# Optimization experiments

Measured on AMD Instinct MI355X. Metric: run time of the kernel, lower is better.

Reference implementation:

```python
import jax, jax.numpy as jnp
import numpy as np

H = 16          # query heads
HKV = 4         # kv heads
DK = 128        # head_qk_dim
DV = 128        # head_v_dim
HID = 2048
KSZ = 4         # conv kernel size
EPS = 1e-5
NORMALIZER = 16.0


def _causal_dwconv_silu(x, w):
    # x: (B,S,C), w: (C,K). Causal depthwise conv then SiLU.
    B, S, C = x.shape
    K = w.shape[1]
    xp = jnp.pad(x, ((0, 0), (K - 1, 0), (0, 0)))
    y = jnp.zeros_like(x)
    for i in range(K):  # K=4, tiny fixed loop
        y = y + w[:, i] * xp[:, i:i + S, :]
    return jax.nn.silu(y)


def _l2norm(x, eps=1e-6):
    return x * jax.lax.rsqrt(jnp.sum(x * x, axis=-1, keepdims=True) + eps)


def setup_inputs() -> dict:
    key = jax.random.key(0)
    ks = jax.random.split(key, 8)
    B, S = 2, 2048
    qkv_dim = H * DK + HKV * DK + HKV * DV  # 3072
    s = lambda fan_in: 1.0 / np.sqrt(fan_in)
    return {
        "hidden_states": jax.random.normal(ks[0], (B, S, HID), jnp.float32),
        "qkv_w": jax.random.uniform(ks[1], (qkv_dim, HID), jnp.float32, -s(HID), s(HID)),
        "g_w": jax.random.uniform(ks[2], (H * DV, HID), jnp.float32, -s(HID), s(HID)),
        "b_w": jax.random.uniform(ks[3], (H, HID), jnp.float32, -s(HID), s(HID)),
        "gk_w": jax.random.uniform(ks[4], (H, HID), jnp.float32, -s(HID), s(HID)),
        "conv_w": jax.random.uniform(ks[5], (qkv_dim, KSZ), jnp.float32, -s(KSZ), s(KSZ)),
        "out_norm_w": jnp.ones((DV,), jnp.float32),
        "o_w": jax.random.uniform(ks[6], (HID, H * DV), jnp.float32, -s(H * DV), s(H * DV)),
    }


def reference(hidden_states, qkv_w, g_w, b_w, gk_w, conv_w, out_norm_w, o_w):
    x = hidden_states
    B, S, _ = x.shape
    grp = H // HKV

    qkv = x @ qkv_w.T                                   # (B,S,3072)
    qkv = _causal_dwconv_silu(qkv, conv_w)
    q, k, v = jnp.split(qkv, [H * DK, H * DK + HKV * DK], axis=-1)
    q = q.reshape(B, S, H, DK)
    k = k.reshape(B, S, HKV, DK)
    v = v.reshape(B, S, HKV, DV)
    # GQA expansion
    k = jnp.repeat(k, grp, axis=2)                      # (B,S,H,DK)
    v = jnp.repeat(v, grp, axis=2)                      # (B,S,H,DV)

    # q/k L2 norm + scale
    q = _l2norm(q) * (DK ** -0.5)
    k = _l2norm(k)

    # decay gate (logsigmoid, log-space), write strength beta
    g_log = jax.nn.log_sigmoid(x @ gk_w.T) / NORMALIZER  # (B,S,H)
    alpha = jnp.exp(g_log)
    beta = jax.nn.sigmoid(x @ b_w.T)                     # (B,S,H)

    # gated delta rule: S_t = a_t*S_{t-1} + k_t (x) beta_t*(v_t - k_t @ (a_t*S_{t-1}))
    def step(Sstate, inp):
        q_t, k_t, v_t, a_t, b_t = inp                    # (B,H,*)
        Sstate = Sstate * a_t[..., None, None]           # (B,H,DK,DV)
        v_pred = jnp.einsum('bhk,bhkv->bhv', k_t, Sstate)
        delta = (v_t - v_pred) * b_t[..., None]
        Sstate = Sstate + jnp.einsum('bhk,bhv->bhkv', k_t, delta)
        o_t = jnp.einsum('bhk,bhkv->bhv', q_t, Sstate)
        return Sstate, o_t

    tfirst = lambda a: jnp.moveaxis(a, 1, 0)             # (S,B,H,...)
    S0 = jnp.zeros((B, H, DK, DV), x.dtype)
    _, o = jax.lax.scan(step, S0, (tfirst(q), tfirst(k), tfirst(v), tfirst(alpha), tfirst(beta)))
    o = jnp.moveaxis(o, 0, 1)                            # (B,S,H,DV)

    # gated per-head RMSNorm then output projection
    g = (x @ g_w.T).reshape(B, S, H, DV)
    o = o * jax.lax.rsqrt(jnp.mean(o * o, axis=-1, keepdims=True) + EPS) * out_norm_w
    o = o * jax.nn.silu(g)
    return (o.reshape(B, S, H * DV)) @ o_w.T
```

## Files before the change

kernel.cpp:

```cpp
#include <hip/hip_runtime.h>
#include <math.h>

#define S_LEN 2048
#define BATCH 2
#define NH 16
#define NKV 4
#define DKQ 128
#define DVV 128
#define HID 2048
#define QKV_DIM 3072
#define M_TOK 4096

typedef _Float16 halfx8 __attribute__((ext_vector_type(8)));
typedef _Float16 halfx4 __attribute__((ext_vector_type(4)));
typedef float floatx4 __attribute__((ext_vector_type(4)));

#define AS1 __attribute__((address_space(1)))
#define AS3 __attribute__((address_space(3)))
#define GLD16(gp, lp) __builtin_amdgcn_global_load_lds((AS1 const void*)(gp), (AS3 void*)(lp), 16, 0, 0)
#define MFMA16(a, b, c) __builtin_amdgcn_mfma_f32_16x16x32_f16(a, b, c, 0, 0, 0)

#define PA_STRIDE 81920

__device__ __forceinline__ float sigmoidf_(float x) { return 1.f / (1.f + __expf(-x)); }

__global__ __launch_bounds__(256) void cvt_f16(const float* __restrict__ in,
                                               _Float16* __restrict__ out, int n8) {
  int i = blockIdx.x * 256 + threadIdx.x;
  if (i >= n8) return;
  const float4* p = (const float4*)in;
  float4 a = p[2 * (size_t)i], b = p[2 * (size_t)i + 1];
  halfx8 o;
  o[0] = (_Float16)a.x; o[1] = (_Float16)a.y; o[2] = (_Float16)a.z; o[3] = (_Float16)a.w;
  o[4] = (_Float16)b.x; o[5] = (_Float16)b.y; o[6] = (_Float16)b.z; o[7] = (_Float16)b.w;
  *(halfx8*)(out + (size_t)i * 8) = o;
}

__global__ __launch_bounds__(256) void gemm_bt_f16(const _Float16* __restrict__ A,
                                                   const _Float16* __restrict__ B,
                                                   float* __restrict__ C,
                                                   int M, int N, int K) {
  __shared__ _Float16 As[128 * 32];
  __shared__ _Float16 Bs[128 * 32];
  int bm = blockIdx.y * 128, bn = blockIdx.x * 128;
  int tid = threadIdx.x;
  int w = tid >> 6, l = tid & 63;
  int wm = (w & 1) * 64, wn = (w >> 1) * 64;
  int lrow = l & 15, lk8 = (l >> 4) * 8;

  floatx4 zero = {0.f, 0.f, 0.f, 0.f};
  floatx4 acc[4][4];
#pragma unroll
  for (int i = 0; i < 4; ++i)
#pragma unroll
    for (int j = 0; j < 4; ++j) acc[i][j] = zero;

  const _Float16* ga = A + (size_t)(bm + (tid >> 2)) * K + (tid & 3) * 8;
  const _Float16* gb = B + (size_t)(bn + (tid >> 2)) * K + (tid & 3) * 8;
  _Float16* lA = As + w * 512;
  _Float16* lB = Bs + w * 512;

  for (int k0 = 0; k0 < K; k0 += 32) {
    GLD16(ga + k0, lA);
    GLD16(ga + k0 + (size_t)64 * K, lA + 2048);
    GLD16(gb + k0, lB);
    GLD16(gb + k0 + (size_t)64 * K, lB + 2048);
    __syncthreads();
    halfx8 af[4], bf_[4];
#pragma unroll
    for (int mi = 0; mi < 4; ++mi)
      af[mi] = *(const halfx8*)&As[(wm + mi * 16 + lrow) * 32 + lk8];
#pragma unroll
    for (int ni = 0; ni < 4; ++ni)
      bf_[ni] = *(const halfx8*)&Bs[(wn + ni * 16 + lrow) * 32 + lk8];
#pragma unroll
    for (int mi = 0; mi < 4; ++mi)
#pragma unroll
      for (int ni = 0; ni < 4; ++ni)
        acc[mi][ni] = MFMA16(af[mi], bf_[ni], acc[mi][ni]);
    __syncthreads();
  }
  int r0 = (l >> 4) * 4;
#pragma unroll
  for (int mi = 0; mi < 4; ++mi)
#pragma unroll
    for (int ni = 0; ni < 4; ++ni) {
      int col = bn + wn + ni * 16 + lrow;
#pragma unroll
      for (int r = 0; r < 4; ++r)
        C[(size_t)(bm + wm + mi * 16 + r0 + r) * N + col] = acc[mi][ni][r];
    }
}

__global__ __launch_bounds__(256) void gkb_kernel(const float* __restrict__ X,
                                                  const float* __restrict__ gk_w,
                                                  const float* __restrict__ b_w,
                                                  float* __restrict__ glog,
                                                  float* __restrict__ be) {
  __shared__ float xs[16][260];
  __shared__ float ws[32][260];
  int tid = threadIdx.x;
  int m0 = blockIdx.x * 16;
  int tl = tid >> 4, n0 = tid & 15;
  float acc0 = 0.f, acc1 = 0.f;
  for (int k0 = 0; k0 < HID; k0 += 256) {
#pragma unroll
    for (int i = 0; i < 4; ++i) {
      int F = i * 256 + tid;
      int r = F >> 6, c4 = (F & 63) * 4;
      *(float4*)&xs[r][c4] = *(const float4*)&X[(size_t)(m0 + r) * HID + k0 + c4];
    }
#pragma unroll
    for (int i = 0; i < 8; ++i) {
      int F = i * 256 + tid;
      int r = F >> 6, c4 = (F & 63) * 4;
      const float* src = (r < 16) ? (gk_w + (size_t)r * HID) : (b_w + (size_t)(r - 16) * HID);
      *(float4*)&ws[r][c4] = *(const float4*)&src[k0 + c4];
    }
    __syncthreads();
#pragma unroll 16
    for (int k = 0; k < 256; k += 4) {
      float4 a = *(const float4*)&xs[tl][k];
      float4 w0 = *(const float4*)&ws[n0][k];
      float4 w1 = *(const float4*)&ws[n0 + 16][k];
      acc0 += a.x * w0.x + a.y * w0.y + a.z * w0.z + a.w * w0.w;
      acc1 += a.x * w1.x + a.y * w1.y + a.z * w1.z + a.w * w1.w;
    }
    __syncthreads();
  }
  int m = m0 + tl, b = m >> 11, s = m & (S_LEN - 1);
  float z = acc0;
  float ls = (z >= 0.f) ? -log1pf(expf(-z)) : (z - log1pf(expf(z)));
  size_t oi = (size_t)(b * NH + n0) * S_LEN + s;
  glog[oi] = ls * 0.0625f;
  be[oi] = sigmoidf_(acc1);
}

__global__ __launch_bounds__(256) void conv_kernel(const float* __restrict__ qkv,
                                                   const float* __restrict__ conv_w,
                                                   float* __restrict__ qn,
                                                   float* __restrict__ kn,
                                                   float* __restrict__ vn) {
  __shared__ float ys[QKV_DIM];
  __shared__ float sc[20];
  int m = blockIdx.x;
  int b = m >> 11, s = m & (S_LEN - 1);
  int tid = threadIdx.x;
  for (int c = tid; c < QKV_DIM; c += 256) {
    float acc = 0.f;
#pragma unroll
    for (int i = 0; i < 4; ++i) {
      int si = s - 3 + i;
      if (si >= 0) acc += conv_w[c * 4 + i] * qkv[(size_t)(b * S_LEN + si) * QKV_DIM + c];
    }
    ys[c] = acc * (1.f / (1.f + __expf(-acc)));
  }
  __syncthreads();
  int wv = tid >> 6, lane = tid & 63;
  for (int ch = wv; ch < 20; ch += 4) {
    int base = (ch < 16) ? ch * 128 : 2048 + (ch - 16) * 128;
    float x0 = ys[base + lane], x1 = ys[base + 64 + lane];
    float ss = x0 * x0 + x1 * x1;
#pragma unroll
    for (int off = 1; off < 64; off <<= 1) ss += __shfl_xor(ss, off);
    float scale = rsqrtf(ss + 1e-6f);
    if (ch < 16) scale *= 0.08838834764831845f;
    if (lane == 0) sc[ch] = scale;
  }
  __syncthreads();
  for (int c = tid; c < 2048; c += 256) {
    int h = c >> 7, d = c & 127;
    qn[((size_t)(b * NH + h) * S_LEN + s) * DKQ + d] = ys[c] * sc[h];
  }
  for (int c = tid; c < 512; c += 256) {
    int j = c >> 7, d = c & 127;
    kn[((size_t)(b * NKV + j) * S_LEN + s) * DKQ + d] = ys[2048 + c] * sc[16 + j];
    vn[((size_t)(b * NKV + j) * S_LEN + s) * DVV + d] = ys[2560 + c];
  }
}

__global__ __launch_bounds__(256, 2) void phaseA_kernel(const float* __restrict__ qn,
                                                        const float* __restrict__ kn,
                                                        const float* __restrict__ vn,
                                                        const float* __restrict__ glog,
                                                        const float* __restrict__ be,
                                                        char* __restrict__ pout,
                                                        float* __restrict__ obuf) {
  __shared__ char smem[80128] __attribute__((aligned(16)));
  _Float16* kh = (_Float16*)smem;
  _Float16* qh = (_Float16*)(smem + 22528);
  float*    LT = (float*)(smem + 45056);
  _Float16* Ph = (_Float16*)(smem + 67584);
  float*    sc_c    = (float*)(smem + 78848);
  float*    sc_beta = sc_c + 64;
  float*    sc_gam  = sc_c + 128;
  float*    sc_bg   = sc_c + 192;
  float*    sc_gcr  = sc_c + 256;
  _Float16* Dt = (_Float16*)smem;
  _Float16* Wt = (_Float16*)(smem + 22528);
  _Float16* Kt = (_Float16*)(smem + 45056);

  int u = blockIdx.x;
  int bh = u >> 5, ch = u & 31;
  int t0 = ch * 64;
  int b = bh >> 4, h = bh & 15, kvh = h >> 2;
  const float* qb = qn + ((size_t)bh * S_LEN + t0) * DKQ;
  const float* kb = kn + (((size_t)(b * NKV + kvh)) * S_LEN + t0) * DKQ;
  const float* vb = vn + (((size_t)(b * NKV + kvh)) * S_LEN + t0) * DVV;
  const float* gl = glog + (size_t)bh * S_LEN + t0;
  const float* ber = be + (size_t)bh * S_LEN + t0;
  char* base = pout + (size_t)u * PA_STRIDE;
  _Float16* M_out = (_Float16*)base;
  _Float16* E_out = (_Float16*)(base + 32768);
  _Float16* B_out = (_Float16*)(base + 49152);
  float* ob = obuf + ((size_t)bh * S_LEN + t0) * DVV;

  int tid = threadIdx.x;
  if (tid < 64) {
    float x = gl[tid];
#pragma unroll
    for (int off = 1; off < 64; off <<= 1) {
      float y = __shfl_up(x, off);
      if (tid >= off) x += y;
    }
    sc_c[tid] = x;
  }
#pragma unroll
  for (int i = 0; i < 8; ++i) {
    int idx = i * 256 + tid;
    int t = idx >> 5, d4 = (idx & 31) * 4;
    float4 kv4 = *(const float4*)&kb[(size_t)t * DKQ + d4];
    float4 qv4 = *(const float4*)&qb[(size_t)t * DKQ + d4];
    _Float16* kd = &kh[t * 152 + d4];
    kd[0] = (_Float16)kv4.x; kd[1] = (_Float16)kv4.y; kd[2] = (_Float16)kv4.z; kd[3] = (_Float16)kv4.w;
    _Float16* qd = &qh[t * 152 + d4];
    qd[0] = (_Float16)qv4.x; qd[1] = (_Float16)qv4.y; qd[2] = (_Float16)qv4.z; qd[3] = (_Float16)qv4.w;
  }
  __syncthreads();
  if (tid < 64) {
    float c = sc_c[tid], c63 = sc_c[63];
    float gam = __expf(c);
    float bet = ber[tid];
    sc_gam[tid] = gam; sc_beta[tid] = bet; sc_bg[tid] = bet * gam;
    sc_gcr[tid] = __expf(c63 - c);
  }
  __syncthreads();

  float z[64];
  {
    const float* src = (tid < 128) ? vb : kb;
    const float* mult = (tid < 128) ? sc_beta : sc_bg;
    int col = tid & 127;
#pragma unroll
    for (int t = 0; t < 64; ++t) z[t] = mult[t] * src[(size_t)t * 128 + col];
  }

  int w = tid >> 6, l = tid & 63;
  int lr = l & 15, lk8 = (l >> 4) * 8, q4 = (l >> 4) * 4;
  floatx4 acc[8];
#pragma unroll
  for (int i = 0; i < 8; ++i) acc[i] = (floatx4){0.f, 0.f, 0.f, 0.f};
#pragma unroll
  for (int job = 0; job < 8; ++job) {
    int j2 = w * 8 + job;
    int tm = (j2 & 15) >> 2, tn = j2 & 3;
    const _Float16* Ar = (j2 < 16) ? kh : qh;
#pragma unroll
    for (int kk = 0; kk < 4; ++kk) {
      halfx8 af = *(const halfx8*)&Ar[(tm * 16 + lr) * 152 + kk * 32 + lk8];
      halfx8 bf = *(const halfx8*)&kh[(tn * 16 + lr) * 152 + kk * 32 + lk8];
      acc[job] = MFMA16(af, bf, acc[job]);
    }
  }
#pragma unroll
  for (int job = 0; job < 8; ++job) {
    int j2 = w * 8 + job;
    int tm = (j2 & 15) >> 2, tn = j2 & 3;
    int jcol = tn * 16 + lr;
    float cj = sc_c[jcol];
#pragma unroll
    for (int r = 0; r < 4; ++r) {
      int trow = tm * 16 + q4 + r;
      float val = acc[job][r] * __expf(sc_c[trow] - cj);
      if (j2 < 16) {
        LT[jcol * 68 + trow] = (jcol < trow) ? sc_beta[trow] * val : 0.f;
      } else {
        Ph[trow * 88 + jcol] = (_Float16)((jcol <= trow) ? val : 0.f);
      }
    }
  }
  __syncthreads();

#pragma unroll
  for (int t = 0; t < 64; ++t) {
    float zt = z[t];
    const int start = ((t + 1) >> 2) << 2;
#pragma unroll
    for (int t2 = start; t2 < 64; t2 += 4) {
      float4 lv = *(const float4*)&LT[t * 68 + t2];
      z[t2 + 0] -= lv.x * zt;
      z[t2 + 1] -= lv.y * zt;
      z[t2 + 2] -= lv.z * zt;
      z[t2 + 3] -= lv.w * zt;
    }
  }
  floatx4 Eacc[8];
#pragma unroll
  for (int ni = 0; ni < 8; ++ni)
#pragma unroll
    for (int r = 0; r < 4; ++r) {
      int trow = w * 16 + q4 + r;
      Eacc[ni][r] = sc_gam[trow] * (float)qh[trow * 152 + ni * 16 + lr];
    }
  __syncthreads();

  {
    int d = tid >> 1, tb = (tid & 1) * 32;
#pragma unroll
    for (int j = 0; j < 4; ++j) {
      halfx8 kv;
#pragma unroll
      for (int r = 0; r < 8; ++r) {
        int t = tb + j * 8 + r;
        kv[r] = (_Float16)(sc_gcr[t] * (float)kh[t * 152 + d]);
      }
      *(halfx8*)&Kt[d * 88 + tb + j * 8] = kv;
    }
  }
  if (tid >= 128) {
    int col = tid & 127;
#pragma unroll
    for (int t = 0; t < 64; t += 8) {
      halfx8 wv;
#pragma unroll
      for (int r = 0; r < 8; ++r) wv[r] = (_Float16)(-z[t + r]);
      *(halfx8*)&Wt[col * 88 + t] = wv;
    }
  }
  __syncthreads();
  if (tid < 128) {
    int col = tid & 127;
#pragma unroll
    for (int t = 0; t < 64; t += 8) {
      halfx8 dv;
#pragma unroll
      for (int r = 0; r < 8; ++r) dv[r] = (_Float16)z[t + r];
      *(halfx8*)&Dt[col * 88 + t] = dv;
    }
  }
  __syncthreads();

  floatx4 Macc[2][8], Bacc[2][8], Oacc[8];
  float gC = __expf(sc_c[63]);
#pragma unroll
  for (int mi = 0; mi < 2; ++mi)
#pragma unroll
    for (int ni = 0; ni < 8; ++ni) {
#pragma unroll
      for (int r = 0; r < 4; ++r)
        Macc[mi][ni][r] = ((w * 32 + mi * 16 + q4 + r) == (ni * 16 + lr)) ? gC : 0.f;
      Bacc[mi][ni] = (floatx4){0.f, 0.f, 0.f, 0.f};
    }
#pragma unroll
  for (int ni = 0; ni < 8; ++ni) Oacc[ni] = (floatx4){0.f, 0.f, 0.f, 0.f};
#pragma unroll
  for (int ks = 0; ks < 2; ++ks) {
    halfx8 ka0 = *(const halfx8*)&Kt[(w * 32 + lr) * 88 + ks * 32 + lk8];
    halfx8 ka1 = *(const halfx8*)&Kt[(w * 32 + 16 + lr) * 88 + ks * 32 + lk8];
    halfx8 pa = *(const halfx8*)&Ph[(w * 16 + lr) * 88 + ks * 32 + lk8];
#pragma unroll
    for (int ni = 0; ni < 8; ++ni) {
      halfx8 wb = *(const halfx8*)&Wt[(ni * 16 + lr) * 88 + ks * 32 + lk8];
      halfx8 db = *(const halfx8*)&Dt[(ni * 16 + lr) * 88 + ks * 32 + lk8];
      Macc[0][ni] = MFMA16(ka0, wb, Macc[0][ni]);
      Macc[1][ni] = MFMA16(ka1, wb, Macc[1][ni]);
      Bacc[0][ni] = MFMA16(ka0, db, Bacc[0][ni]);
      Bacc[1][ni] = MFMA16(ka1, db, Bacc[1][ni]);
      Eacc[ni] = MFMA16(pa, wb, Eacc[ni]);
      Oacc[ni] = MFMA16(pa, db, Oacc[ni]);
    }
  }
#pragma unroll
  for (int mi = 0; mi < 2; ++mi)
#pragma unroll
    for (int ni = 0; ni < 8; ++ni)
#pragma unroll
      for (int r = 0; r < 4; ++r) {
        int row = w * 32 + mi * 16 + q4 + r;
        M_out[row * 128 + ni * 16 + lr] = (_Float16)Macc[mi][ni][r];
        B_out[ni * 2048 + row * 16 + lr] = (_Float16)Bacc[mi][ni][r];
      }
#pragma unroll
  for (int ni = 0; ni < 8; ++ni)
#pragma unroll
    for (int r = 0; r < 4; ++r) {
      int trow = w * 16 + q4 + r;
      E_out[trow * 128 + ni * 16 + lr] = (_Float16)Eacc[ni][r];
      ob[(size_t)trow * 128 + ni * 16 + lr] = Oacc[ni][r];
    }
}

__global__ __launch_bounds__(256, 1) void phaseB_kernel(const char* __restrict__ pin,
                                                        float* __restrict__ obuf) {
  __shared__ _Float16 Mh[2][128 * 152];
  __shared__ _Float16 Eh[2][64 * 152];
  __shared__ _Float16 St[2][16 * 152];

  int bh = blockIdx.x & 31, vg = blockIdx.x >> 5;
  int tid = threadIdx.x, w = tid >> 6, l = tid & 63;
  int lr = l & 15, lk8 = (l >> 4) * 8, q4 = (l >> 4) * 4;
  const char* ub0 = pin + (size_t)(bh * 32) * PA_STRIDE;
  float* ob_base = obuf + (size_t)bh * S_LEN * DVV + vg * 16;

  float4 Mr[8], Er[4];
  float Bc[2][4], Oc[4], Bn[2][4], On[4];

  {
    const float4* Mg = (const float4*)ub0;
    const float4* Eg = (const float4*)(ub0 + 32768);
    const _Float16* Bg = (const _Float16*)(ub0 + 49152) + vg * 2048;
#pragma unroll
    for (int j = 0; j < 8; ++j) Mr[j] = Mg[j * 256 + tid];
#pragma unroll
    for (int j = 0; j < 4; ++j) Er[j] = Eg[j * 256 + tid];
#pragma unroll
    for (int mi = 0; mi < 2; ++mi)
#pragma unroll
      for (int r = 0; r < 4; ++r)
        Bc[mi][r] = (float)Bg[(w * 32 + mi * 16 + q4 + r) * 16 + lr];
#pragma unroll
    for (int r = 0; r < 4; ++r)
      Oc[r] = ob_base[(size_t)(w * 16 + q4 + r) * DVV + lr];
#pragma unroll
    for (int j = 0; j < 8; ++j) {
      int n = j * 256 + tid;
      *(float4*)&Mh[0][(n >> 4) * 152 + (n & 15) * 8] = Mr[j];
    }
#pragma unroll
    for (int j = 0; j < 4; ++j) {
      int n = j * 256 + tid;
      *(float4*)&Eh[0][(n >> 4) * 152 + (n & 15) * 8] = Er[j];
    }
    halfx4 z4;
    z4[0] = (_Float16)0.f; z4[1] = (_Float16)0.f; z4[2] = (_Float16)0.f; z4[3] = (_Float16)0.f;
#pragma unroll
    for (int mi = 0; mi < 2; ++mi)
      *(halfx4*)&St[0][lr * 152 + w * 32 + mi * 16 + q4] = z4;
  }
  asm volatile("s_waitcnt lgkmcnt(0)" ::: "memory");

  for (int c = 0; c < 32; ++c) {
    __builtin_amdgcn_s_barrier();
    int cur = c & 1, nxt = cur ^ 1;
    bool have = (c + 1) < 32;
    if (have) {
      const char* un = ub0 + (size_t)(c + 1) * PA_STRIDE;
      const float4* Mg = (const float4*)un;
      const float4* Eg = (const float4*)(un + 32768);
      const _Float16* Bg = (const _Float16*)(un + 49152) + vg * 2048;
#pragma unroll
      for (int j = 0; j < 8; ++j) Mr[j] = Mg[j * 256 + tid];
#pragma unroll
      for (int j = 0; j < 4; ++j) Er[j] = Eg[j * 256 + tid];
#pragma unroll
      for (int mi = 0; mi < 2; ++mi)
#pragma unroll
        for (int r = 0; r < 4; ++r)
          Bn[mi][r] = (float)Bg[(w * 32 + mi * 16 + q4 + r) * 16 + lr];
#pragma unroll
      for (int r = 0; r < 4; ++r)
        On[r] = ob_base[(size_t)((c + 1) * 64 + w * 16 + q4 + r) * DVV + lr];
    }
    floatx4 Sn0 = {Bc[0][0], Bc[0][1], Bc[0][2], Bc[0][3]};
    floatx4 Sn1 = {Bc[1][0], Bc[1][1], Bc[1][2], Bc[1][3]};
    floatx4 Oa = {Oc[0], Oc[1], Oc[2], Oc[3]};
#pragma unroll
    for (int ks = 0; ks < 4; ++ks) {
      halfx8 sf = *(const halfx8*)&St[cur][lr * 152 + ks * 32 + lk8];
      halfx8 ma0 = *(const halfx8*)&Mh[cur][(w * 32 + lr) * 152 + ks * 32 + lk8];
      halfx8 ma1 = *(const halfx8*)&Mh[cur][(w * 32 + 16 + lr) * 152 + ks * 32 + lk8];
      halfx8 ea = *(const halfx8*)&Eh[cur][(w * 16 + lr) * 152 + ks * 32 + lk8];
      Sn0 = MFMA16(ma0, sf, Sn0);
      Sn1 = MFMA16(ma1, sf, Sn1);
      Oa = MFMA16(ea, sf, Oa);
    }
    {
      float* obr = ob_base + (size_t)c * 64 * DVV;
#pragma unroll
      for (int r = 0; r < 4; ++r)
        obr[(size_t)(w * 16 + q4 + r) * DVV + lr] = Oa[r];
    }
#pragma unroll
    for (int mi = 0; mi < 2; ++mi) {
      halfx4 sv;
      floatx4 Sm = mi ? Sn1 : Sn0;
#pragma unroll
      for (int r = 0; r < 4; ++r) sv[r] = (_Float16)Sm[r];
      *(halfx4*)&St[nxt][lr * 152 + w * 32 + mi * 16 + q4] = sv;
    }
    if (have) {
#pragma unroll
      for (int j = 0; j < 8; ++j) {
        int n = j * 256 + tid;
        *(float4*)&Mh[nxt][(n >> 4) * 152 + (n & 15) * 8] = Mr[j];
      }
#pragma unroll
      for (int j = 0; j < 4; ++j) {
        int n = j * 256 + tid;
        *(float4*)&Eh[nxt][(n >> 4) * 152 + (n & 15) * 8] = Er[j];
      }
#pragma unroll
      for (int mi = 0; mi < 2; ++mi)
#pragma unroll
        for (int r = 0; r < 4; ++r) Bc[mi][r] = Bn[mi][r];
#pragma unroll
      for (int r = 0; r < 4; ++r) Oc[r] = On[r];
    }
    asm volatile("s_waitcnt lgkmcnt(0)" ::: "memory");
  }
}

__global__ __launch_bounds__(256) void normgate_kernel(const float* __restrict__ o_buf,
                                                       const float* __restrict__ g_buf,
                                                       const float* __restrict__ nw,
                                                       _Float16* __restrict__ og) {
  int gid = blockIdx.x * 4 + (threadIdx.x >> 6);
  int lane = threadIdx.x & 63;
  int m = gid >> 4, h = gid & 15;
  int b = m >> 11, s = m & (S_LEN - 1);
  const float* orow = o_buf + ((size_t)(b * NH + h) * S_LEN + s) * DVV;
  float o0 = orow[lane], o1 = orow[lane + 64];
  float ss = o0 * o0 + o1 * o1;
#pragma unroll
  for (int off = 1; off < 64; off <<= 1) ss += __shfl_xor(ss, off);
  float r = rsqrtf(ss * (1.f / 128.f) + 1e-5f);
  size_t gi = (size_t)m * HID + h * DVV;
  float g0 = g_buf[gi + lane], g1 = g_buf[gi + lane + 64];
  og[gi + lane] = (_Float16)(o0 * r * nw[lane] * (g0 * sigmoidf_(g0)));
  og[gi + lane + 64] = (_Float16)(o1 * r * nw[lane + 64] * (g1 * sigmoidf_(g1)));
}

extern "C" void kernel_launch(void* const* d_in, const int* in_sizes, int n_in,
                              void* d_out, int out_size, void* d_ws, size_t ws_size,
                              hipStream_t stream) {
  const float* X      = (const float*)d_in[0];
  const float* qkv_w  = (const float*)d_in[1];
  const float* g_w    = (const float*)d_in[2];
  const float* b_w    = (const float*)d_in[3];
  const float* gk_w   = (const float*)d_in[4];
  const float* conv_w = (const float*)d_in[5];
  const float* norm_w = (const float*)d_in[6];
  const float* o_w    = (const float*)d_in[7];
  float* out = (float*)d_out;

  char* ws = (char*)d_ws;
  float* qkv_buf   = (float*)(ws);
  float* g_buf     = (float*)(ws);
  _Float16* ow16   = (_Float16*)(ws + 33554432);
  float* glog      = (float*)(ws + 41943040);
  float* be        = (float*)(ws + 42205184);
  float* qn        = (float*)(ws + 50331648);
  float* kn        = (float*)(ws + 83886080);
  float* vn        = (float*)(ws + 92274688);
  _Float16* X16    = (_Float16*)(ws + 100663296);
  _Float16* qw16   = (_Float16*)(ws + 117440512);
  _Float16* gw16   = (_Float16*)(ws + 130023424);
  char*  pA        = (char*)(ws + 100663296);
  _Float16* og16   = (_Float16*)(ws + 100663296);
  float* o_buf     = qn;

  dim3 blk(256);
  cvt_f16<<<dim3(4096), blk, 0, stream>>>(X, X16, 1048576);
  cvt_f16<<<dim3(3072), blk, 0, stream>>>(qkv_w, qw16, 786432);
  cvt_f16<<<dim3(2048), blk, 0, stream>>>(g_w, gw16, 524288);
  gemm_bt_f16<<<dim3(QKV_DIM / 128, M_TOK / 128), blk, 0, stream>>>(X16, qw16, qkv_buf, M_TOK, QKV_DIM, HID);
  conv_kernel<<<dim3(M_TOK), blk, 0, stream>>>(qkv_buf, conv_w, qn, kn, vn);
  gkb_kernel<<<dim3(M_TOK / 16), blk, 0, stream>>>(X, gk_w, b_w, glog, be);
  cvt_f16<<<dim3(2048), blk, 0, stream>>>(o_w, ow16, 524288);
  gemm_bt_f16<<<dim3(HID / 128, M_TOK / 128), blk, 0, stream>>>(X16, gw16, g_buf, M_TOK, HID, HID);
  phaseA_kernel<<<dim3(1024), blk, 0, stream>>>(qn, kn, vn, glog, be, pA, o_buf);
  phaseB_kernel<<<dim3(256), blk, 0, stream>>>(pA, o_buf);
  normgate_kernel<<<dim3(M_TOK * NH / 4), blk, 0, stream>>>(o_buf, g_buf, norm_w, og16);
  gemm_bt_f16<<<dim3(HID / 128, M_TOK / 128), blk, 0, stream>>>(og16, ow16, out, M_TOK, HID, HID);
}
```

Baseline: 530.3 us.

## Replace GEMM with 256x256 double-buffered 8-wave MFMA kernel with swizzled LDS

Replaces the 128x128 single-buffered fp16 GEMM with a 512-thread, 256x256-tile kernel using K=64 steps, double-buffered direct-to-LDS loads, XOR-swizzled LDS layout, and interleaved ds_read/MFMA phases with s_setprio. It also remaps block IDs for L2 locality. The aim is to hide global load latency and raise MFMA utilization. The large tiles reduce the grid to 128-192 workgroups, which may leave many CUs idle, and the kernel uses 128KB of LDS.

```diff
diff --git a/kernel.cpp b/kernel.cpp
--- a/kernel.cpp
+++ b/kernel.cpp
@@ -19,6 +19,7 @@
 #define AS3 __attribute__((address_space(3)))
 #define GLD16(gp, lp) __builtin_amdgcn_global_load_lds((AS1 const void*)(gp), (AS3 void*)(lp), 16, 0, 0)
 #define MFMA16(a, b, c) __builtin_amdgcn_mfma_f32_16x16x32_f16(a, b, c, 0, 0, 0)
+#define SBAR() asm volatile("s_barrier" ::: "memory")
 
 #define PA_STRIDE 81920
 
@@ -36,60 +37,156 @@
   *(halfx8*)(out + (size_t)i * 8) = o;
 }
 
-__global__ __launch_bounds__(256) void gemm_bt_f16(const _Float16* __restrict__ A,
-                                                   const _Float16* __restrict__ B,
-                                                   float* __restrict__ C,
-                                                   int M, int N, int K) {
-  __shared__ _Float16 As[128 * 32];
-  __shared__ _Float16 Bs[128 * 32];
-  int bm = blockIdx.y * 128, bn = blockIdx.x * 128;
-  int tid = threadIdx.x;
-  int w = tid >> 6, l = tid & 63;
-  int wm = (w & 1) * 64, wn = (w >> 1) * 64;
-  int lrow = l & 15, lk8 = (l >> 4) * 8;
-
-  floatx4 zero = {0.f, 0.f, 0.f, 0.f};
-  floatx4 acc[4][4];
-#pragma unroll
-  for (int i = 0; i < 4; ++i)
-#pragma unroll
-    for (int j = 0; j < 4; ++j) acc[i][j] = zero;
-
-  const _Float16* ga = A + (size_t)(bm + (tid >> 2)) * K + (tid & 3) * 8;
-  const _Float16* gb = B + (size_t)(bn + (tid >> 2)) * K + (tid & 3) * 8;
-  _Float16* lA = As + w * 512;
-  _Float16* lB = Bs + w * 512;
-
-  for (int k0 = 0; k0 < K; k0 += 32) {
-    GLD16(ga + k0, lA);
-    GLD16(ga + k0 + (size_t)64 * K, lA + 2048);
-    GLD16(gb + k0, lB);
-    GLD16(gb + k0 + (size_t)64 * K, lB + 2048);
-    __syncthreads();
-    halfx8 af[4], bf_[4];
+__global__ __launch_bounds__(512, 2) void gemm_bt_f16_8ph(const _Float16* __restrict__ A,
+                                                          const _Float16* __restrict__ B,
+                                                          float* __restrict__ C,
+                                                          int M, int N, int K) {
+  __shared__ char lds[131072] __attribute__((aligned(16)));
+  const int tid = threadIdx.x;
+  const int wid = tid >> 6, l = tid & 63;
+  const int lr = l & 15, hi = l >> 4;
+  const int wm = wid >> 2, wn = wid & 3;
+
+  int nbx = gridDim.x;
+  int bid = blockIdx.y * nbx + blockIdx.x;
+  int nwg = nbx * gridDim.y;
+  int swz = (nwg & 7) ? bid : ((bid & 7) * (nwg >> 3) + (bid >> 3));
+  int bm = (swz / nbx) * 256, bn = (swz % nbx) * 256;
+
+  const int srow = wid * 8 + (l >> 3);
+  const int csrc = ((l & 7) ^ (((l >> 5) & 1) << 1)) * 8;
+  const _Float16* ga[4];
+  const _Float16* gb[4];
+#pragma unroll
+  for (int h = 0; h < 2; ++h)
+#pragma unroll
+    for (int j = 0; j < 2; ++j) {
+      int r = h * 128 + j * 64 + srow;
+      ga[h * 2 + j] = A + (size_t)(bm + r) * K + csrc;
+      gb[h * 2 + j] = B + (size_t)(bn + r) * K + csrc;
+    }
+  int soff[8];
+#pragma unroll
+  for (int h = 0; h < 2; ++h)
+#pragma unroll
+    for (int j = 0; j < 2; ++j) {
+      soff[h * 2 + j] = h * 16384 + j * 8192 + (wid << 10);
+      soff[4 + h * 2 + j] = 32768 + h * 16384 + j * 8192 + (wid << 10);
+    }
+
+  const int sw2 = ((lr >> 2) & 1) << 1;
+  int cA[2];
+  cA[0] = ((0 * 4 + hi) ^ sw2) * 16;
+  cA[1] = ((1 * 4 + hi) ^ sw2) * 16;
+  const int abase = wm * 16384 + lr * 128;
+  int bbase[4];
+#pragma unroll
+  for (int ni = 0; ni < 4; ++ni) {
+    int rowN = wn * 64 + ni * 16 + lr;
+    bbase[ni] = 32768 + (rowN >> 7) * 16384 + (rowN & 127) * 128;
+  }
+
+  floatx4 acc[8][4];
+#pragma unroll
+  for (int i = 0; i < 8; ++i)
+#pragma unroll
+    for (int j = 0; j < 4; ++j) acc[i][j] = (floatx4){0.f, 0.f, 0.f, 0.f};
+
+  const int NT = K >> 6;
+#define STAGE8(tt, pp)                                           \
+  {                                                              \
+    int kof = (tt) * 64;                                         \
+    int pof = (pp) * 65536;                                      \
+    _Pragma("unroll") for (int q = 0; q < 4; ++q) {              \
+      GLD16(ga[q] + kof, lds + pof + soff[q]);                   \
+      GLD16(gb[q] + kof, lds + pof + soff[4 + q]);               \
+    }                                                            \
+  }
+
+  STAGE8(0, 0);
+  asm volatile("s_waitcnt vmcnt(0)" ::: "memory");
+  SBAR();
+
+  halfx8 af[4][2], bf[4][2];
+  for (int t = 0; t < NT; ++t) {
+    const char* bufc = lds + (t & 1) * 65536;
+    if (t + 1 < NT) STAGE8(t + 1, (t + 1) & 1);
 #pragma unroll
     for (int mi = 0; mi < 4; ++mi)
-      af[mi] = *(const halfx8*)&As[(wm + mi * 16 + lrow) * 32 + lk8];
-#pragma unroll
-    for (int ni = 0; ni < 4; ++ni)
-      bf_[ni] = *(const halfx8*)&Bs[(wn + ni * 16 + lrow) * 32 + lk8];
+#pragma unroll
+      for (int ks = 0; ks < 2; ++ks)
+        af[mi][ks] = *(const halfx8*)(bufc + abase + mi * 2048 + cA[ks]);
+#pragma unroll
+    for (int ni = 0; ni < 2; ++ni)
+#pragma unroll
+      for (int ks = 0; ks < 2; ++ks)
+        bf[ni][ks] = *(const halfx8*)(bufc + bbase[ni] + cA[ks]);
+    SBAR();
+    __builtin_amdgcn_s_setprio(1);
 #pragma unroll
     for (int mi = 0; mi < 4; ++mi)
 #pragma unroll
-      for (int ni = 0; ni < 4; ++ni)
-        acc[mi][ni] = MFMA16(af[mi], bf_[ni], acc[mi][ni]);
-    __syncthreads();
-  }
-  int r0 = (l >> 4) * 4;
-#pragma unroll
-  for (int mi = 0; mi < 4; ++mi)
+      for (int ni = 0; ni < 2; ++ni)
+#pragma unroll
+        for (int ks = 0; ks < 2; ++ks)
+          acc[mi][ni] = MFMA16(af[mi][ks], bf[ni][ks], acc[mi][ni]);
+    __builtin_amdgcn_s_setprio(0);
+    SBAR();
+#pragma unroll
+    for (int ni = 2; ni < 4; ++ni)
+#pragma unroll
+      for (int ks = 0; ks < 2; ++ks)
+        bf[ni][ks] = *(const halfx8*)(bufc + bbase[ni] + cA[ks]);
+    SBAR();
+    __builtin_amdgcn_s_setprio(1);
+#pragma unroll
+    for (int mi = 0; mi < 4; ++mi)
+#pragma unroll
+      for (int ni = 2; ni < 4; ++ni)
+#pragma unroll
+        for (int ks = 0; ks < 2; ++ks)
+          acc[mi][ni] = MFMA16(af[mi][ks], bf[ni][ks], acc[mi][ni]);
+    __builtin_amdgcn_s_setprio(0);
+    SBAR();
+#pragma unroll
+    for (int mi = 0; mi < 4; ++mi)
+#pragma unroll
+      for (int ks = 0; ks < 2; ++ks)
+        af[mi][ks] = *(const halfx8*)(bufc + abase + (mi + 4) * 2048 + cA[ks]);
+    SBAR();
+    __builtin_amdgcn_s_setprio(1);
+#pragma unroll
+    for (int mi = 0; mi < 4; ++mi)
+#pragma unroll
+      for (int ni = 2; ni < 4; ++ni)
+#pragma unroll
+        for (int ks = 0; ks < 2; ++ks)
+          acc[mi + 4][ni] = MFMA16(af[mi][ks], bf[ni][ks], acc[mi + 4][ni]);
+    __builtin_amdgcn_s_setprio(0);
+    SBAR();
+    __builtin_amdgcn_s_setprio(1);
+#pragma unroll
+    for (int mi = 0; mi < 4; ++mi)
+#pragma unroll
+      for (int ni = 0; ni < 2; ++ni)
+#pragma unroll
+        for (int ks = 0; ks < 2; ++ks)
+          acc[mi + 4][ni] = MFMA16(af[mi][ks], bf[ni][ks], acc[mi + 4][ni]);
+    __builtin_amdgcn_s_setprio(0);
+    asm volatile("s_waitcnt vmcnt(0)" ::: "memory");
+    SBAR();
+  }
+#pragma unroll
+  for (int mi = 0; mi < 8; ++mi)
 #pragma unroll
     for (int ni = 0; ni < 4; ++ni) {
-      int col = bn + wn + ni * 16 + lrow;
+      int row0 = bm + wm * 128 + mi * 16 + hi * 4;
+      int col = bn + wn * 64 + ni * 16 + lr;
 #pragma unroll
       for (int r = 0; r < 4; ++r)
-        C[(size_t)(bm + wm + mi * 16 + r0 + r) * N + col] = acc[mi][ni][r];
-    }
+        C[(size_t)(row0 + r) * N + col] = acc[mi][ni][r];
+    }
+#undef STAGE8
 }
 
 __global__ __launch_bounds__(256) void gkb_kernel(const float* __restrict__ X,
@@ -570,16 +667,17 @@
   float* o_buf     = qn;
 
   dim3 blk(256);
+  dim3 blk512(512);
   cvt_f16<<<dim3(4096), blk, 0, stream>>>(X, X16, 1048576);
   cvt_f16<<<dim3(3072), blk, 0, stream>>>(qkv_w, qw16, 786432);
   cvt_f16<<<dim3(2048), blk, 0, stream>>>(g_w, gw16, 524288);
-  gemm_bt_f16<<<dim3(QKV_DIM / 128, M_TOK / 128), blk, 0, stream>>>(X16, qw16, qkv_buf, M_TOK, QKV_DIM, HID);
+  gemm_bt_f16_8ph<<<dim3(QKV_DIM / 256, M_TOK / 256), blk512, 0, stream>>>(X16, qw16, qkv_buf, M_TOK, QKV_DIM, HID);
   conv_kernel<<<dim3(M_TOK), blk, 0, stream>>>(qkv_buf, conv_w, qn, kn, vn);
   gkb_kernel<<<dim3(M_TOK / 16), blk, 0, stream>>>(X, gk_w, b_w, glog, be);
   cvt_f16<<<dim3(2048), blk, 0, stream>>>(o_w, ow16, 524288);
-  gemm_bt_f16<<<dim3(HID / 128, M_TOK / 128), blk, 0, stream>>>(X16, gw16, g_buf, M_TOK, HID, HID);
+  gemm_bt_f16_8ph<<<dim3(HID / 256, M_TOK / 256), blk512, 0, stream>>>(X16, gw16, g_buf, M_TOK, HID, HID);
   phaseA_kernel<<<dim3(1024), blk, 0, stream>>>(qn, kn, vn, glog, be, pA, o_buf);
   phaseB_kernel<<<dim3(256), blk, 0, stream>>>(pA, o_buf);
   normgate_kernel<<<dim3(M_TOK * NH / 4), blk, 0, stream>>>(o_buf, g_buf, norm_w, og16);
-  gemm_bt_f16<<<dim3(HID / 128, M_TOK / 128), blk, 0, stream>>>(og16, ow16, out, M_TOK, HID, HID);
-}
+  gemm_bt_f16_8ph<<<dim3(HID / 256, M_TOK / 256), blk512, 0, stream>>>(og16, ow16, out, M_TOK, HID, HID);
+}
```

Result: no change. 537.8 us (+1.4%).
